# Optimization experiments

Measured on AMD Instinct MI355X. Metric: run time of the kernel, lower is better.

Reference implementation:

```python
import jax, jax.numpy as jnp
import numpy as np
import math

B, S, D = 2, 2048, 4096
H, KVH, HD = 32, 8, 128
N_REP = H // KVH
HALF = HD // 2
ROPE_THETA = 500000.0


def _rope(t, cos, sin):
    # t: [b, s, h, hd]; cos/sin: [s, hd/2]
    tr = t.reshape(t.shape[:-1] + (HALF, 2))
    a, b = tr[..., 0], tr[..., 1]
    c = cos[None, :, None, :]
    s = sin[None, :, None, :]
    ra = a * c - b * s
    rb = a * s + b * c
    return jnp.stack([ra, rb], axis=-1).reshape(t.shape)


def setup_inputs() -> dict:
    key = jax.random.key(0)
    ks = jax.random.split(key, 5)
    x = jax.random.normal(ks[0], (B, S, D), jnp.float32)
    wq = jax.random.normal(ks[1], (D, H * HD), jnp.float32) * 0.02
    wk = jax.random.normal(ks[2], (D, KVH * HD), jnp.float32) * 0.02
    wv = jax.random.normal(ks[3], (D, KVH * HD), jnp.float32) * 0.02
    wo = jax.random.normal(ks[4], (H * HD, D), jnp.float32) * 0.02
    inv_freq = 1.0 / (ROPE_THETA ** (jnp.arange(HALF, dtype=jnp.float32) / HALF))
    pos = jnp.arange(S, dtype=jnp.float32)
    ang = pos[:, None] * inv_freq[None, :]  # [S, HD/2]
    freqs_cos = jnp.cos(ang)
    freqs_sin = jnp.sin(ang)
    # multiplicative causal mask (source does scores * mask)
    mask = jnp.tril(jnp.ones((S, S), jnp.float32))
    cache_k = jnp.zeros((B, S, KVH, HD), jnp.float32)
    cache_v = jnp.zeros((B, S, KVH, HD), jnp.float32)
    return {
        "x": x, "freqs_cos": freqs_cos, "freqs_sin": freqs_sin, "mask": mask,
        "wq": wq, "wk": wk, "wv": wv, "wo": wo,
        "cache_k": cache_k, "cache_v": cache_v, "start_pos": 0,
    }


def reference(x, freqs_cos, freqs_sin, mask, wq, wk, wv, wo, cache_k, cache_v, start_pos):
    bsz, seqlen, _ = x.shape
    xq = (x @ wq).reshape(bsz, seqlen, H, HD)
    xk = (x @ wk).reshape(bsz, seqlen, KVH, HD)
    xv = (x @ wv).reshape(bsz, seqlen, KVH, HD)
    xq = _rope(xq, freqs_cos, freqs_sin)
    xk = _rope(xk, freqs_cos, freqs_sin)
    # KV cache append
    cache_k = jax.lax.dynamic_update_slice(cache_k, xk, (0, start_pos, 0, 0))
    cache_v = jax.lax.dynamic_update_slice(cache_v, xv, (0, start_pos, 0, 0))
    kv_len = start_pos + seqlen
    keys = cache_k[:bsz, :kv_len]      # [b, kv, kvh, hd]
    values = cache_v[:bsz, :kv_len]
    # GQA: repeat kv heads
    keys = jnp.repeat(keys, N_REP, axis=2)    # [b, kv, h, hd]
    values = jnp.repeat(values, N_REP, axis=2)
    scores = jnp.einsum('bqhd,bkhd->bhqk', xq, keys) / math.sqrt(HD)
    scores = scores * mask[:seqlen, :kv_len]  # multiplicative mask (as in source)
    scores = jax.nn.softmax(scores.astype(jnp.float32), axis=-1).astype(xq.dtype)
    out = jnp.einsum('bhqk,bkhd->bqhd', scores, values)
    out = out.reshape(bsz, seqlen, H * HD)
    return out @ wo
```

## Files before the change

### kernel.cpp

```cpp
#include <hip/hip_runtime.h>
#include <hip/hip_bf16.h>

typedef __bf16 bf16;
typedef bf16 bf16x8 __attribute__((ext_vector_type(8)));
typedef bf16 bf16x4 __attribute__((ext_vector_type(4)));
typedef bf16 bf16x2 __attribute__((ext_vector_type(2)));
typedef float f32x4 __attribute__((ext_vector_type(4)));

#define MFMA16(a, b, c) __builtin_amdgcn_mfma_f32_16x16x32_bf16(a, b, c, 0, 0, 0)

constexpr int BB = 2, SS = 2048, DD = 4096, HH = 32, KVHH = 8, HDD = 128;
constexpr int QDIM = HH * HDD;
constexpr int KVDIM = KVHH * HDD;
constexpr int NQKV = QDIM + 2 * KVDIM;
constexpr int LDX = NQKV;

__device__ inline void gload16(const bf16* g, bf16* l) {
    __builtin_amdgcn_global_load_lds((const __attribute__((address_space(1))) void*)g,
                                     (__attribute__((address_space(3))) void*)l, 16, 0, 0);
}

union U32BF2 { unsigned int u; bf16x2 v; };

__global__ __launch_bounds__(256) void cvt_bf16(const float* __restrict__ src,
                                                bf16* __restrict__ dst, int n4) {
    int i = blockIdx.x * 256 + threadIdx.x;
    if (i >= n4) return;
    float4 v = ((const float4*)src)[i];
    bf16x4 o;
    o[0] = (bf16)v.x; o[1] = (bf16)v.y; o[2] = (bf16)v.z; o[3] = (bf16)v.w;
    ((bf16x4*)dst)[i] = o;
}

__global__ __launch_bounds__(256) void transpose_w(const float* __restrict__ src,
                                                   bf16* __restrict__ dst, int R, int C) {
    __shared__ bf16 t[32][33];
    int tx = threadIdx.x & 31, ty = threadIdx.x >> 5;
    int r0 = blockIdx.y * 32, c0 = blockIdx.x * 32;
#pragma unroll
    for (int i = 0; i < 4; i++)
        t[ty + i * 8][tx] = (bf16)src[(long)(r0 + ty + i * 8) * C + c0 + tx];
    __syncthreads();
#pragma unroll
    for (int i = 0; i < 4; i++)
        dst[(long)(c0 + ty + i * 8) * R + r0 + tx] = t[tx][ty + i * 8];
}

__global__ __launch_bounds__(256) void transpose_v(const bf16* __restrict__ XQKV,
                                                   bf16* __restrict__ Vt) {
    __shared__ bf16 t[32][33];
    int z = blockIdx.z, b = z >> 3, kvh = z & 7;
    int h0 = blockIdx.x * 32, p0 = blockIdx.y * 32;
    int tx = threadIdx.x & 31, ty = threadIdx.x >> 5;
#pragma unroll
    for (int i = 0; i < 4; i++)
        t[ty + i * 8][tx] = XQKV[(long)(b * SS + p0 + ty + i * 8) * LDX + QDIM + KVDIM +
                                 kvh * HDD + h0 + tx];
    __syncthreads();
#pragma unroll
    for (int i = 0; i < 4; i++)
        Vt[((long)(b * KVHH + kvh) * HDD + h0 + ty + i * 8) * SS + p0 + tx] =
            t[tx][ty + i * 8];
}

__global__ __launch_bounds__(256) void rope_q(bf16* __restrict__ X,
                                              const float* __restrict__ fc,
                                              const float* __restrict__ fs) {
    const float c2 = 0.08838834764831845f * 1.4426950408889634f;
    long t = (long)blockIdx.x * 256 + threadIdx.x;
    int i2 = (int)(t & 63);
    long u = t >> 6;
    int hh = (int)(u & 31);
    long bp = u >> 5;
    int pos = (int)(bp & (SS - 1));
    unsigned int* p = (unsigned int*)&X[bp * LDX + hh * HDD + 2 * i2];
    U32BF2 cv; cv.u = *p;
    float a = (float)cv.v[0], bb = (float)cv.v[1];
    float c = fc[pos * 64 + i2], s = fs[pos * 64 + i2];
    U32BF2 o;
    o.v[0] = (bf16)((a * c - bb * s) * c2);
    o.v[1] = (bf16)((a * s + bb * c) * c2);
    *p = o.u;
}

__global__ __launch_bounds__(256) void rope_kc(const bf16* __restrict__ X,
                                               const float* __restrict__ fc,
                                               const float* __restrict__ fs,
                                               bf16* __restrict__ Kc) {
    long t = (long)blockIdx.x * 256 + threadIdx.x;
    int i2 = (int)(t & 63);
    long u = t >> 6;
    int pos = (int)(u & (SS - 1));
    int bk = (int)(u >> 11);
    int b = bk >> 3, kvh = bk & 7;
    const unsigned int* p =
        (const unsigned int*)&X[((long)(b * SS) + pos) * LDX + QDIM + kvh * HDD + 2 * i2];
    U32BF2 cv; cv.u = *p;
    float a = (float)cv.v[0], bb = (float)cv.v[1];
    float c = fc[pos * 64 + i2], s = fs[pos * 64 + i2];
    U32BF2 o;
    o.v[0] = (bf16)(a * c - bb * s);
    o.v[1] = (bf16)(a * s + bb * c);
    ((unsigned int*)Kc)[u * 64 + i2] = o.u;
}

__global__ __launch_bounds__(256) void sufv_k(const bf16* __restrict__ Vt,
                                              float* __restrict__ Suf) {
    __shared__ float ts[128][33];
    int bk = blockIdx.x;
    int hd = threadIdx.x & 127, tg = threadIdx.x >> 7;
    const bf16* row = Vt + ((long)bk * HDD + hd) * SS;
#pragma unroll
    for (int tt = 0; tt < 16; tt++) {
        int t = tg * 16 + tt;
        const bf16* p = row + t * 64;
        float s = 0.f;
#pragma unroll
        for (int j = 0; j < 8; j++) {
            bf16x8 v = *(const bf16x8*)&p[j * 8];
#pragma unroll
            for (int e = 0; e < 8; e++) s += (float)v[e];
        }
        ts[hd][t] = s;
    }
    __syncthreads();
    if (threadIdx.x < 128) {
        int h2 = threadIdx.x;
        float run = 0.f;
        Suf[((long)bk * 33 + 32) * HDD + h2] = 0.f;
        for (int t = 31; t >= 1; t--) {
            run += ts[h2][t];
            Suf[((long)bk * 33 + t) * HDD + h2] = run;
        }
    }
}

template <typename CT>
__global__ __launch_bounds__(256) void gemm_bt(const bf16* __restrict__ A,
                                               const bf16* __restrict__ BT,
                                               CT* __restrict__ C, int M, int N, int K) {
    __shared__ bf16 As[128 * 32];
    __shared__ bf16 Bs[128 * 32];
    const int tid = threadIdx.x;
    const int lane = tid & 63, w = tid >> 6;
    const int quad = lane >> 4, lcol = lane & 15;
    const int m0 = blockIdx.y * 128, n0 = blockIdx.x * 128;
    const int wm = (w >> 1) * 64, wn = (w & 1) * 64;
    const int sr = tid >> 2;
    const int sc = (tid & 3) * 8;
    const bf16* ga = &A[(long)(m0 + sr) * K + sc];
    const bf16* gb = &BT[(long)(n0 + sr) * K + sc];
    bf16* lA = &As[w * 512];
    bf16* lB = &Bs[w * 512];
    f32x4 acc[4][4] = {};

    for (int k0 = 0; k0 < K; k0 += 32) {
        gload16(ga + k0, lA);
        gload16(ga + (long)64 * K + k0, lA + 2048);
        gload16(gb + k0, lB);
        gload16(gb + (long)64 * K + k0, lB + 2048);
        __syncthreads();
        bf16x8 af[4], bfr[4];
#pragma unroll
        for (int i = 0; i < 4; i++)
            af[i] = *(const bf16x8*)&As[(wm + i * 16 + lcol) * 32 + quad * 8];
#pragma unroll
        for (int j = 0; j < 4; j++)
            bfr[j] = *(const bf16x8*)&Bs[(wn + j * 16 + lcol) * 32 + quad * 8];
#pragma unroll
        for (int i = 0; i < 4; i++)
#pragma unroll
            for (int j = 0; j < 4; j++) acc[i][j] = MFMA16(af[i], bfr[j], acc[i][j]);
        __syncthreads();
    }
#pragma unroll
    for (int i = 0; i < 4; i++)
#pragma unroll
        for (int j = 0; j < 4; j++)
#pragma unroll
            for (int r = 0; r < 4; r++) {
                int row = m0 + wm + i * 16 + quad * 4 + r;
                int col = n0 + wn + j * 16 + lcol;
                C[(long)row * N + col] = (CT)acc[i][j][r];
            }
}

__global__ __launch_bounds__(512, 4) void attn_k(const bf16* __restrict__ XQKV,
                                                 const bf16* __restrict__ Kc,
                                                 const bf16* __restrict__ Vt,
                                                 const float* __restrict__ Suf,
                                                 bf16* __restrict__ AO) {
    __shared__ bf16 Ks[2][64 * 128];
    __shared__ bf16 Vs[2][128 * 64];
    __shared__ bf16 Pl[8][16 * 64];
    const int tid = threadIdx.x;
    const int lane = tid & 63, w = tid >> 6;
    const int quad = lane >> 4, lcol = lane & 15;
    const int h = blockIdx.y, b = blockIdx.z;
    const int kvh = h >> 2;

    const bf16* KcB = Kc + (long)((b * KVHH + kvh) * SS) * HDD;
    const bf16* VtB = Vt + (long)((b * KVHH + kvh) * HDD) * SS;

    int kofs[2], vofs[2];
#pragma unroll
    for (int i = 0; i < 2; i++) {
        int j = i * 512 + tid;
        int p = j >> 4, cp = j & 15, c = cp ^ (p & 7);
        kofs[i] = p * HDD + c * 8;
        int r = j >> 3, cp2 = j & 7, cv = cp2 ^ (r & 7);
        vofs[i] = r * SS + cv * 8;
    }

    auto stageKV = [&](int buf, int kb0s) {
        bf16* ksb = &Ks[buf][0];
        bf16* vsb = &Vs[buf][0];
#pragma unroll
        for (int i = 0; i < 2; i++)
            gload16(KcB + (long)kb0s * HDD + kofs[i], &ksb[(i * 512 + tid) * 8]);
#pragma unroll
        for (int i = 0; i < 2; i++)
            gload16(VtB + (long)kb0s + vofs[i], &vsb[(i * 512 + tid) * 8]);
    };

    for (int rep = 0; rep < 2; rep++) {
        const int qc = rep == 0 ? 15 - (int)blockIdx.x : (int)blockIdx.x;
        const int qbase = qc * 128 + w * 16;
        const int NT = 2 * qc + 2;
        const int qpos = qbase + lcol;

        bf16x8 qf[4];
#pragma unroll
        for (int kc = 0; kc < 4; kc++)
            qf[kc] = *(const bf16x8*)&XQKV[((long)(b * SS) + qbase + lcol) * LDX +
                                           h * HDD + kc * 32 + quad * 8];
        f32x4 oacc[8] = {};
        float m2 = -1e30f, l = 0.f;

        stageKV(0, 0);
        asm volatile("s_waitcnt vmcnt(0)" ::: "memory");
        __builtin_amdgcn_s_barrier();

        int cur = 0;
        for (int kt = 0; kt < NT; kt++) {
            const int kb0 = kt * 64;
            stageKV(cur ^ 1, (kt + 1 < NT ? kt + 1 : kt) * 64);

            const bf16* KsC = &Ks[cur][0];
            const bf16* VsC = &Vs[cur][0];
            f32x4 sa[4] = {};
            __builtin_amdgcn_s_setprio(1);
#pragma unroll
            for (int ch = 0; ch < 4; ch++) {
                int p = ch * 16 + lcol;
#pragma unroll
                for (int kc = 0; kc < 4; kc++) {
                    int c = kc * 4 + quad;
                    bf16x8 kf = *(const bf16x8*)&KsC[(p * 16 + (c ^ (p & 7))) * 8];
                    sa[ch] = MFMA16(kf, qf[kc], sa[ch]);
                }
            }
            __builtin_amdgcn_s_setprio(0);
            if (kb0 + 63 > qbase) {
#pragma unroll
                for (int ch = 0; ch < 4; ch++)
#pragma unroll
                    for (int r = 0; r < 4; r++)
                        if (kb0 + ch * 16 + quad * 4 + r > qpos) sa[ch][r] = 0.f;
            }
            f32x4 mx = sa[0];
#pragma unroll
            for (int ch = 1; ch < 4; ch++)
#pragma unroll
                for (int r = 0; r < 4; r++) mx[r] = fmaxf(mx[r], sa[ch][r]);
            float mt = fmaxf(fmaxf(mx[0], mx[1]), fmaxf(mx[2], mx[3]));
            mt = fmaxf(mt, __shfl_xor(mt, 16, 64));
            mt = fmaxf(mt, __shfl_xor(mt, 32, 64));
            float mnew = fmaxf(m2, mt);
            float alpha = exp2f(m2 - mnew);
            m2 = mnew;
            float rs = 0.f;
            const int xm = (lcol & 7) << 3;
            bf16* plw = &Pl[w][0];
#pragma unroll
            for (int ch = 0; ch < 4; ch++) {
                bf16x4 pv;
#pragma unroll
                for (int r = 0; r < 4; r++) {
                    float e = exp2f(sa[ch][r] - mnew);
                    rs += e;
                    pv[r] = (bf16)e;
                }
                *(bf16x4*)&plw[lcol * 64 + ((ch * 16 + quad * 4) ^ xm)] = pv;
            }
            l = l * alpha + rs;
            bf16x8 pf0 = *(const bf16x8*)&plw[lcol * 64 + ((quad * 8) ^ xm)];
            bf16x8 pf1 = *(const bf16x8*)&plw[lcol * 64 + ((32 + quad * 8) ^ xm)];
            float a4[4];
#pragma unroll
            for (int r = 0; r < 4; r++)
                a4[r] = __shfl(alpha, (quad << 4) | (quad * 4 + r), 64);
            __builtin_amdgcn_s_setprio(1);
#pragma unroll
            for (int nj = 0; nj < 8; nj++) {
                int rr = nj * 16 + lcol;
                bf16x8 vf0 = *(const bf16x8*)&VsC[(rr * 8 + (quad ^ (rr & 7))) * 8];
                bf16x8 vf1 = *(const bf16x8*)&VsC[(rr * 8 + ((4 + quad) ^ (rr & 7))) * 8];
                f32x4 o = oacc[nj];
#pragma unroll
                for (int r = 0; r < 4; r++) o[r] *= a4[r];
                o = MFMA16(pf0, vf0, o);
                o = MFMA16(pf1, vf1, o);
                oacc[nj] = o;
            }
            __builtin_amdgcn_s_setprio(0);
            asm volatile("s_waitcnt vmcnt(0)" ::: "memory");
            __builtin_amdgcn_s_barrier();
            cur ^= 1;
        }
        l += __shfl_xor(l, 16, 64);
        l += __shfl_xor(l, 32, 64);
        const int cnt = SS - NT * 64;
        float mf = (cnt > 0) ? fmaxf(m2, 0.f) : m2;
        float so = exp2f(m2 - mf);
        float sm = exp2f(-mf);
        float rz = 1.f / (l * so + (float)cnt * sm);
        float so4[4], sm4[4], rz4[4];
#pragma unroll
        for (int r = 0; r < 4; r++) {
            int src = (quad << 4) | (quad * 4 + r);
            so4[r] = __shfl(so, src, 64);
            sm4[r] = __shfl(sm, src, 64);
            rz4[r] = __shfl(rz, src, 64);
        }
        const float* sufp = &Suf[((long)((b * KVHH + kvh) * 33) + NT) * HDD];
#pragma unroll
        for (int nj = 0; nj < 8; nj++) {
            float suf = sufp[nj * 16 + lcol];
#pragma unroll
            for (int r = 0; r < 4; r++) {
                float o = (oacc[nj][r] * so4[r] + sm4[r] * suf) * rz4[r];
                AO[((long)(b * SS) + qbase + quad * 4 + r) * QDIM + h * HDD +
                   nj * 16 + lcol] = (bf16)o;
            }
        }
    }
}

extern "C" void kernel_launch(void* const* d_in, const int* in_sizes, int n_in,
                              void* d_out, int out_size, void* d_ws, size_t ws_size,
                              hipStream_t stream) {
    const float* x  = (const float*)d_in[0];
    const float* fc = (const float*)d_in[1];
    const float* fs = (const float*)d_in[2];
    const float* wq = (const float*)d_in[4];
    const float* wk = (const float*)d_in[5];
    const float* wv = (const float*)d_in[6];
    const float* wo = (const float*)d_in[7];
    float* out = (float*)d_out;

    char* ws = (char*)d_ws;
    bf16* Wt   = (bf16*)ws; ws += (long)NQKV * DD * 2;
    bf16* woT  = (bf16*)ws; ws += (long)DD * QDIM * 2;
    bf16* XQKV = (bf16*)ws; ws += (long)BB * SS * NQKV * 2;
    bf16* Vt   = (bf16*)ws; ws += (long)BB * KVHH * HDD * SS * 2;
    bf16* Xb   = (bf16*)ws; ws += (long)BB * SS * DD * 2;
    float* Suf = (float*)ws; ws += (long)BB * KVHH * 33 * HDD * 4;
    bf16* AO = Xb;
    bf16* Kc = Wt;

    const int M = BB * SS;

    cvt_bf16<<<(DD * M / 4 + 255) / 256, 256, 0, stream>>>(x, Xb, DD * M / 4);

    transpose_w<<<dim3(QDIM / 32, DD / 32), 256, 0, stream>>>(wq, Wt, DD, QDIM);
    transpose_w<<<dim3(KVDIM / 32, DD / 32), 256, 0, stream>>>(wk, Wt + (long)QDIM * DD, DD, KVDIM);
    transpose_w<<<dim3(KVDIM / 32, DD / 32), 256, 0, stream>>>(wv, Wt + (long)(QDIM + KVDIM) * DD, DD, KVDIM);
    transpose_w<<<dim3(DD / 32, QDIM / 32), 256, 0, stream>>>(wo, woT, QDIM, DD);

    gemm_bt<bf16><<<dim3(NQKV / 128, M / 128), 256, 0, stream>>>(Xb, Wt, XQKV, M, NQKV, DD);

    rope_q<<<(int)(((long)BB * SS * HH * 64) / 256), 256, 0, stream>>>(XQKV, fc, fs);
    rope_kc<<<(int)(((long)BB * KVHH * SS * 64) / 256), 256, 0, stream>>>(XQKV, fc, fs, Kc);

    transpose_v<<<dim3(HDD / 32, SS / 32, BB * KVHH), 256, 0, stream>>>(XQKV, Vt);
    sufv_k<<<BB * KVHH, 256, 0, stream>>>(Vt, Suf);

    attn_k<<<dim3(8, HH, BB), 512, 0, stream>>>(XQKV, Kc, Vt, Suf, AO);

    gemm_bt<float><<<dim3(DD / 128, M / 128), 256, 0, stream>>>(AO, woT, out, M, DD, QDIM);
}
```

Baseline: 926.4 us.

## Replace GEMM with triple-buffered 128x256 tile kernel with swizzled LDS

Replaces the simple synchronous GEMM with a kernel that uses 512 threads, 128x256 output tiles and a three-stage LDS ring filled by direct global-to-LDS loads two tiles ahead. It adds an XOR swizzle on LDS columns, a block-ID remap that groups blocks into 8 chunks, and raised wave priority around the MFMA burst. The goal is to overlap global memory latency with matrix math and cut bank conflicts and barrier stalls in both projection GEMMs. In exchange it uses more LDS and relies on hand-placed waitcnt counts, which must match the number of loads in flight.

Result: faster. 837.6 us (-9.6%).

```diff
diff --git a/kernel.cpp b/kernel.cpp
--- a/kernel.cpp
+++ b/kernel.cpp
@@ -136,42 +136,70 @@
 }
 
 template <typename CT>
-__global__ __launch_bounds__(256) void gemm_bt(const bf16* __restrict__ A,
-                                               const bf16* __restrict__ BT,
-                                               CT* __restrict__ C, int M, int N, int K) {
-    __shared__ bf16 As[128 * 32];
-    __shared__ bf16 Bs[128 * 32];
+__global__ __launch_bounds__(512, 4) void gemm3s(const bf16* __restrict__ A,
+                                                 const bf16* __restrict__ BT,
+                                                 CT* __restrict__ C, int M, int N, int K) {
+    constexpr int BM = 128, BN = 256, BK = 32;
+    constexpr int ASZ = BM * BK;
+    constexpr int BSZ = BN * BK;
+    constexpr int STG = ASZ + BSZ;
+    __shared__ bf16 LDS[3 * STG];
     const int tid = threadIdx.x;
     const int lane = tid & 63, w = tid >> 6;
     const int quad = lane >> 4, lcol = lane & 15;
-    const int m0 = blockIdx.y * 128, n0 = blockIdx.x * 128;
-    const int wm = (w >> 1) * 64, wn = (w & 1) * 64;
-    const int sr = tid >> 2;
-    const int sc = (tid & 3) * 8;
-    const bf16* ga = &A[(long)(m0 + sr) * K + sc];
-    const bf16* gb = &BT[(long)(n0 + sr) * K + sc];
-    bf16* lA = &As[w * 512];
-    bf16* lB = &Bs[w * 512];
+    const int gx = gridDim.x;
+    int bid = blockIdx.y * gx + blockIdx.x;
+    const int cpx = (gx * gridDim.y) >> 3;
+    bid = (bid & 7) * cpx + (bid >> 3);
+    const int m0 = (bid / gx) * BM, n0 = (bid % gx) * BN;
+    const int wm = (w >> 2) * 64, wn = (w & 3) * 64;
+    const int arow = tid >> 2, ac = (tid & 3) ^ (arow & 3);
+    const int brow1 = (tid + 512) >> 2, bc1 = ((tid + 512) & 3) ^ (brow1 & 3);
+    const bf16* gA = &A[(long)(m0 + arow) * K + ac * 8];
+    const bf16* gB0 = &BT[(long)(n0 + arow) * K + ac * 8];
+    const bf16* gB1 = &BT[(long)(n0 + brow1) * K + bc1 * 8];
+    const int xs = (quad ^ (lcol & 3)) * 8;
+    const int aro = (wm + lcol) * BK + xs;
+    const int bro = (wn + lcol) * BK + xs;
+    const int NKT = K / BK;
     f32x4 acc[4][4] = {};
 
-    for (int k0 = 0; k0 < K; k0 += 32) {
-        gload16(ga + k0, lA);
-        gload16(ga + (long)64 * K + k0, lA + 2048);
-        gload16(gb + k0, lB);
-        gload16(gb + (long)64 * K + k0, lB + 2048);
-        __syncthreads();
+    auto stage = [&](int t) {
+        const int bo = (t % 3) * STG;
+        const long ko = (long)t * BK;
+        gload16(gA + ko, &LDS[bo + tid * 8]);
+        gload16(gB0 + ko, &LDS[bo + ASZ + tid * 8]);
+        gload16(gB1 + ko, &LDS[bo + ASZ + (512 + tid) * 8]);
+    };
+
+    stage(0);
+    stage(1);
+    asm volatile("s_waitcnt vmcnt(3)" ::: "memory");
+    __builtin_amdgcn_s_barrier();
+    asm volatile("" ::: "memory");
+
+    for (int t = 0; t < NKT; ++t) {
+        const int bo = (t % 3) * STG;
+        const bf16* la = &LDS[bo + aro];
+        const bf16* lb = &LDS[bo + ASZ + bro];
         bf16x8 af[4], bfr[4];
 #pragma unroll
+        for (int i = 0; i < 4; i++) af[i] = *(const bf16x8*)&la[i * 16 * BK];
+#pragma unroll
+        for (int j = 0; j < 4; j++) bfr[j] = *(const bf16x8*)&lb[j * 16 * BK];
+        if (t + 2 < NKT) stage(t + 2);
+        asm volatile("s_waitcnt lgkmcnt(0)" ::: "memory");
+        __builtin_amdgcn_sched_barrier(0);
+        __builtin_amdgcn_s_setprio(1);
+#pragma unroll
         for (int i = 0; i < 4; i++)
-            af[i] = *(const bf16x8*)&As[(wm + i * 16 + lcol) * 32 + quad * 8];
-#pragma unroll
-        for (int j = 0; j < 4; j++)
-            bfr[j] = *(const bf16x8*)&Bs[(wn + j * 16 + lcol) * 32 + quad * 8];
-#pragma unroll
-        for (int i = 0; i < 4; i++)
 #pragma unroll
             for (int j = 0; j < 4; j++) acc[i][j] = MFMA16(af[i], bfr[j], acc[i][j]);
-        __syncthreads();
+        __builtin_amdgcn_s_setprio(0);
+        if (t + 2 < NKT) asm volatile("s_waitcnt vmcnt(3)" ::: "memory");
+        else             asm volatile("s_waitcnt vmcnt(0)" ::: "memory");
+        __builtin_amdgcn_s_barrier();
+        asm volatile("" ::: "memory");
     }
 #pragma unroll
     for (int i = 0; i < 4; i++)
@@ -378,7 +406,7 @@
     transpose_w<<<dim3(KVDIM / 32, DD / 32), 256, 0, stream>>>(wv, Wt + (long)(QDIM + KVDIM) * DD, DD, KVDIM);
     transpose_w<<<dim3(DD / 32, QDIM / 32), 256, 0, stream>>>(wo, woT, QDIM, DD);
 
-    gemm_bt<bf16><<<dim3(NQKV / 128, M / 128), 256, 0, stream>>>(Xb, Wt, XQKV, M, NQKV, DD);
+    gemm3s<bf16><<<dim3(NQKV / 256, M / 128), 512, 0, stream>>>(Xb, Wt, XQKV, M, NQKV, DD);
 
     rope_q<<<(int)(((long)BB * SS * HH * 64) / 256), 256, 0, stream>>>(XQKV, fc, fs);
     rope_kc<<<(int)(((long)BB * KVHH * SS * 64) / 256), 256, 0, stream>>>(XQKV, fc, fs, Kc);
@@ -388,5 +416,5 @@
 
     attn_k<<<dim3(8, HH, BB), 512, 0, stream>>>(XQKV, Kc, Vt, Suf, AO);
 
-    gemm_bt<float><<<dim3(DD / 128, M / 128), 256, 0, stream>>>(AO, woT, out, M, DD, QDIM);
-}
+    gemm3s<float><<<dim3(DD / 256, M / 128), 512, 0, stream>>>(AO, woT, out, M, DD, QDIM);
+}
```
